# Performance work log

Measured on AMD Instinct MI355X. Metric: run time of the kernel, lower is better.

Reference implementation:

```python
import jax, jax.numpy as jnp
import numpy as np

D = 512          # feature dim
N = 4095         # context length
LMBD = 0.9       # eligibility-trace decay
DIM = 2 * D + 1  # 1025
CTX = N + 1      # 4096


def make_M(n: int, lmbd: float) -> jnp.ndarray:
    # M[row, col] = lmbd**(row-col) for col <= row < n, col < n; last row and
    # last column are all zero (M[-1, -1] explicitly zeroed in the original).
    i = jnp.arange(n, dtype=jnp.int32)
    diff = i[:, None] - i[None, :]
    core = jnp.where(diff >= 0, jnp.float32(lmbd) ** jnp.maximum(diff, 0).astype(jnp.float32), 0.0)
    M = jnp.zeros((n + 1, n + 1), dtype=jnp.float32)
    return M.at[:n, :n].set(core)


def setup_inputs() -> dict:
    key = jax.random.key(0)
    kz, kp, kq = jax.random.split(key, 3)
    Z = jax.random.normal(kz, (DIM, CTX), dtype=jnp.float32)
    # nn.Parameter(torch.empty(...)) is uninitialized in the source; use small
    # random values as stand-ins for trained parameters.
    P = jax.random.normal(kp, (DIM, DIM), dtype=jnp.float32) * 0.02
    Q = jax.random.normal(kq, (DIM, DIM), dtype=jnp.float32) * 0.02
    M = make_M(N, LMBD)
    return {"Z": Z, "P": P, "Q": Q, "M": M}


def reference(Z, P, Q, M):
    # X = Z^T Q Z : (CTX, CTX) bilinear attention scores
    X = jnp.einsum("dn,de,em->nm", Z, Q, Z)
    A = jax.nn.softmax(X, axis=-1)          # activation
    # Z + (1/n) * P @ Z @ M @ A ; contract left-to-right to keep (DIM, CTX) intermediates
    PZ = P @ Z                               # (DIM, CTX)
    PZM = PZ @ M                             # (DIM, CTX), M lower-tri decay
    return Z + (1.0 / N) * (PZM @ A)
```

## Files before the change

kernel.cpp:

```cpp
#include <hip/hip_runtime.h>


#define LMBD 0.9f
#define CTXN 4096
#define DIMN 1025
#define DP 1152

#define KSPLIT 832
#define PSTRIDE ((size_t)DP * CTXN)

typedef __bf16 bf16x8 __attribute__((ext_vector_type(8)));
typedef float f32x4 __attribute__((ext_vector_type(4)));
typedef long lx2 __attribute__((ext_vector_type(2)));

__device__ __forceinline__ unsigned short f2bf(float f) {
  union { float f; unsigned u; } v; v.f = f;
  unsigned r = v.u + 0x7FFFu + ((v.u >> 16) & 1u);
  return (unsigned short)(r >> 16);
}
__device__ __forceinline__ float bf2f(unsigned short h) {
  union { unsigned u; float f; } v; v.u = ((unsigned)h) << 16;
  return v.f;
}

__device__ __forceinline__ void gld_lds16(const void* g, void* l) {
  __builtin_amdgcn_global_load_lds(
      (const __attribute__((address_space(1))) unsigned int*)g,
      (__attribute__((address_space(3))) unsigned int*)l, 16, 0, 0);
}

template <int MODE, int TM, int TN>
__device__ __forceinline__ void gemm_body(
    const unsigned short* __restrict__ A, const unsigned short* __restrict__ B,
    void* __restrict__ Cout, int K, int lda, int ldb, int ldc, int bi, int bj,
    float* __restrict__ pmax, float* __restrict__ psum) {
  constexpr int CA = TM / 16, CB = TN / 16;
  constexpr int FI = TM / 32, FJ = TN / 32;
  __shared__ unsigned short sA[TM * 32];
  __shared__ unsigned short sB[TN * 32];
  const int tid = threadIdx.x;
  const int wave = tid >> 6;
  const int lane = tid & 63;
  const long i0 = (long)bi * TM;
  const long j0 = (long)bj * TN;
  const int wm = (wave & 1) * (TM / 2);
  const int wn = (wave >> 1) * (TN / 2);

  f32x4 acc[FI][FJ] = {};

  const int srow = lane >> 2;
  const int skc = (((lane & 3) - (lane >> 3)) & 3) * 8;
  const int mrow = lane & 15;
  const int slot = ((((lane >> 4) + (mrow >> 1)) & 3)) * 8;

  for (int k0 = 0; k0 < K; k0 += 32) {
    __syncthreads();
#pragma unroll
    for (int c = 0; c < CA / 4; ++c) {
      const int q = wave * (CA / 4) + c;
      gld_lds16(A + (i0 + q * 16 + srow) * (long)lda + k0 + skc, &sA[q * 512]);
    }
#pragma unroll
    for (int c = 0; c < CB / 4; ++c) {
      const int q = wave * (CB / 4) + c;
      gld_lds16(B + (j0 + q * 16 + srow) * (long)ldb + k0 + skc, &sB[q * 512]);
    }
    __syncthreads();
    bf16x8 af[FI], bfr[FJ];
#pragma unroll
    for (int i = 0; i < FI; ++i)
      af[i] = *(const bf16x8*)&sA[(wm + i * 16 + mrow) * 32 + slot];
#pragma unroll
    for (int j = 0; j < FJ; ++j)
      bfr[j] = *(const bf16x8*)&sB[(wn + j * 16 + mrow) * 32 + slot];
#pragma unroll
    for (int i = 0; i < FI; ++i)
#pragma unroll
      for (int j = 0; j < FJ; ++j)
        acc[i][j] =
            __builtin_amdgcn_mfma_f32_16x16x32_bf16(af[i], bfr[j], acc[i][j], 0, 0, 0);
  }

  const int lr = (lane >> 4) * 4;
  const int lc = lane & 15;
#pragma unroll
  for (int i = 0; i < FI; ++i) {
#pragma unroll
    for (int j = 0; j < FJ; ++j) {
#pragma unroll
      for (int r = 0; r < 4; ++r) {
        const long row = i0 + wm + i * 16 + lr + r;
        const long col = j0 + wn + j * 16 + lc;
        const float v = acc[i][j][r];
        if (MODE == 1) ((float*)Cout)[row * ldc + col] = v;
        else ((unsigned short*)Cout)[row * ldc + col] = f2bf(v);
      }
    }
  }

  if (MODE == 4) {
    float* sMax = (float*)sA;
    float* sSum = (float*)sB;
    const int k8 = (wave & 1) * 4 + (lane >> 4);
    __syncthreads();
#pragma unroll
    for (int j = 0; j < FJ; ++j) {
      float m = -1e30f;
#pragma unroll
      for (int i = 0; i < FI; ++i)
#pragma unroll
        for (int r = 0; r < 4; ++r) m = fmaxf(m, acc[i][j][r]);
      float s = 0.f;
#pragma unroll
      for (int i = 0; i < FI; ++i)
#pragma unroll
        for (int r = 0; r < 4; ++r) s += __expf(acc[i][j][r] - m);
      const int c = wn + j * 16 + lc;
      sMax[c * 8 + k8] = m;
      sSum[c * 8 + k8] = s;
    }
    __syncthreads();
    if (tid < 128) {
      float m = -1e30f;
#pragma unroll
      for (int k = 0; k < 8; ++k) m = fmaxf(m, sMax[tid * 8 + k]);
      float s = 0.f;
#pragma unroll
      for (int k = 0; k < 8; ++k) s += sSum[tid * 8 + k] * __expf(sMax[tid * 8 + k] - m);
      pmax[(size_t)bi * CTXN + j0 + tid] = m;
      psum[(size_t)bi * CTXN + j0 + tid] = s;
    }
  }
}

__global__ __launch_bounds__(256, 2) void gemm_xt(
    const unsigned short* __restrict__ QZT, const unsigned short* __restrict__ ZbT,
    unsigned short* __restrict__ XT, float* __restrict__ pmax,
    float* __restrict__ psum) {
  gemm_body<4, 128, 128>(QZT, ZbT, XT, DP, DP, DP, CTXN, blockIdx.x, blockIdx.y, pmax,
                         psum);
}

__global__ __launch_bounds__(256, 2) void gemm_dual(
    const unsigned short* __restrict__ ZbT, const unsigned short* __restrict__ Qb,
    unsigned short* __restrict__ QZT, const unsigned short* __restrict__ Pb,
    float* __restrict__ PZ) {
  const unsigned g = blockIdx.x;
  if (g < 576) {
    gemm_body<0, 128, 64>(ZbT, Qb, QZT, DP, DP, DP, DP, g & 31, g >> 5, nullptr,
                          nullptr);
  } else {
    const unsigned h = g - 576;
    gemm_body<1, 64, 128>(Pb, ZbT, PZ, DP, DP, DP, CTXN, h >> 5, h & 31, nullptr,
                          nullptr);
  }
}

__global__ __launch_bounds__(256, 2) void gemm_fp8_splitk(
    const unsigned char* __restrict__ A, const unsigned char* __restrict__ B,
    unsigned short* __restrict__ Cout) {
  __shared__ unsigned char sA[128 * 64];
  __shared__ unsigned char sB[128 * 64];
  const int tid = threadIdx.x;
  const int wave = tid >> 6;
  const int lane = tid & 63;
  const unsigned g = blockIdx.x;
  const unsigned bi = g / 160;
  const unsigned rem = g % 160;
  const unsigned bj = rem / 5;
  const unsigned bz = rem % 5;
  const long i0 = (long)bi * 128;
  const long j0 = (long)bj * 128;
  const int wm = (wave & 1) * 64;
  const int wn = (wave >> 1) * 64;
  const int kb = bz * KSPLIT;
  const int ke = min(CTXN, kb + KSPLIT);
  Cout += (size_t)bz * PSTRIDE;

  f32x4 acc[4][4] = {};
  const int srow = lane >> 2;
  const int skc = (((lane & 3) - (lane >> 3)) & 3) * 16;
  const int mrow = lane & 15;
  const int slot = ((((lane >> 4) + (mrow >> 1)) & 3)) * 16;

  for (int k0 = kb; k0 < ke; k0 += 64) {
    __syncthreads();
#pragma unroll
    for (int c = 0; c < 2; ++c) {
      const int q = wave * 2 + c;
      gld_lds16(A + (i0 + q * 16 + srow) * (long)CTXN + k0 + skc, &sA[q * 1024]);
      gld_lds16(B + (j0 + q * 16 + srow) * (long)CTXN + k0 + skc, &sB[q * 1024]);
    }
    __syncthreads();
    lx2 af[4], bfr[4];
#pragma unroll
    for (int i = 0; i < 4; ++i)
      af[i] = *(const lx2*)&sA[(wm + i * 16 + mrow) * 64 + slot];
#pragma unroll
    for (int j = 0; j < 4; ++j)
      bfr[j] = *(const lx2*)&sB[(wn + j * 16 + mrow) * 64 + slot];
#pragma unroll
    for (int i = 0; i < 4; ++i)
#pragma unroll
      for (int j = 0; j < 4; ++j) {
        acc[i][j] = __builtin_amdgcn_mfma_f32_16x16x32_fp8_fp8(af[i].x, bfr[j].x,
                                                               acc[i][j], 0, 0, 0);
        acc[i][j] = __builtin_amdgcn_mfma_f32_16x16x32_fp8_fp8(af[i].y, bfr[j].y,
                                                               acc[i][j], 0, 0, 0);
      }
  }

  const int lr = (lane >> 4) * 4;
  const int lc = lane & 15;
#pragma unroll
  for (int i = 0; i < 4; ++i)
#pragma unroll
    for (int j = 0; j < 4; ++j)
#pragma unroll
      for (int r = 0; r < 4; ++r) {
        const long row = i0 + wm + i * 16 + lr + r;
        if (row < DIMN)
          Cout[row * (long)CTXN + j0 + wn + j * 16 + lc] = f2bf(acc[i][j][r]);
      }
}

__global__ void reduce_kernel(const unsigned short* __restrict__ Pt,
                              const float* __restrict__ Z, float* __restrict__ out) {
  const size_t idx = ((size_t)blockIdx.x * 256 + threadIdx.x) * 4;
  float ax = 0.f, ay = 0.f, az = 0.f, aw = 0.f;
#pragma unroll
  for (int z = 0; z < 5; ++z) {
    const ushort4 v = *(const ushort4*)&Pt[(size_t)z * PSTRIDE + idx];
    ax += bf2f(v.x); ay += bf2f(v.y); az += bf2f(v.z); aw += bf2f(v.w);
  }
  const f32x4 zv = *(const f32x4*)&Z[idx];
  f32x4 o;
  o[0] = zv[0] + ax * 0.00390625f;
  o[1] = zv[1] + ay * 0.00390625f;
  o[2] = zv[2] + az * 0.00390625f;
  o[3] = zv[3] + aw * 0.00390625f;
  *(f32x4*)&out[idx] = o;
}

__global__ void pad_kernel(const float* __restrict__ Q, const float* __restrict__ P,
                           unsigned short* __restrict__ Qb,
                           unsigned short* __restrict__ Pb) {
  const int c = blockIdx.x * 128 + threadIdx.x;
  const int r = blockIdx.y;
  const float* src = blockIdx.z ? P : Q;
  unsigned short* dst = blockIdx.z ? Pb : Qb;
  float v = (r < DIMN && c < DIMN) ? src[(size_t)r * DIMN + c] : 0.f;
  dst[(size_t)r * DP + c] = f2bf(v);
}

__global__ void transZ_kernel(const float* __restrict__ Z, unsigned short* __restrict__ ZbT) {
  __shared__ float tile[32][33];
  const int n0 = blockIdx.x * 32, e0 = blockIdx.y * 32;
  const int tx = threadIdx.x, ty = threadIdx.y;
#pragma unroll
  for (int k = 0; k < 4; ++k) {
    const int e = e0 + ty + k * 8;
    tile[ty + k * 8][tx] = (e < DIMN) ? Z[(size_t)e * CTXN + n0 + tx] : 0.f;
  }
  __syncthreads();
#pragma unroll
  for (int k = 0; k < 4; ++k) {
    const int n = n0 + ty + k * 8;
    ZbT[(size_t)n * DP + e0 + tx] = f2bf(tile[tx][ty + k * 8]);
  }
}

__global__ void red2_kernel(const float* __restrict__ pmax, const float* __restrict__ psum,
                            float* __restrict__ rowmax, float* __restrict__ inv_l) {
  const int n = blockIdx.x * 256 + threadIdx.x;
  float M = -1e30f;
  for (int c = 0; c < 32; ++c) M = fmaxf(M, pmax[(size_t)c * CTXN + n]);
  float s = 0.f;
  for (int c = 0; c < 32; ++c)
    s += psum[(size_t)c * CTXN + n] * __expf(pmax[(size_t)c * CTXN + n] - M);
  rowmax[n] = M;
  inv_l[n] = 1.0f / (4095.0f * s);
}

__global__ void ew_kernel(const unsigned short* __restrict__ XT,
                          const float* __restrict__ rowmax, unsigned int* __restrict__ ET) {
  const size_t idx = ((size_t)blockIdx.x * 256 + threadIdx.x) * 4;
  const ushort4 v = *(const ushort4*)&XT[idx];
  const int n = (int)(idx & 4095);
  const float4 rm = *(const float4*)&rowmax[n];
  unsigned p = __builtin_amdgcn_cvt_pk_fp8_f32(__expf(bf2f(v.x) - rm.x),
                                               __expf(bf2f(v.y) - rm.y), 0, false);
  p = __builtin_amdgcn_cvt_pk_fp8_f32(__expf(bf2f(v.z) - rm.z),
                                      __expf(bf2f(v.w) - rm.w), p, true);
  ET[idx >> 2] = p;
}

__global__ __launch_bounds__(256) void scan_kernel(const float* __restrict__ PZ,
                                                   const float* __restrict__ inv_l,
                                                   unsigned char* __restrict__ out) {
  const int d = blockIdx.x;
  const int t = threadIdx.x;
  const float* row = PZ + (size_t)d * CTXN;
  float x[16];
#pragma unroll
  for (int q = 0; q < 4; ++q) {
    const float4 v = *(const float4*)&row[t * 16 + q * 4];
    x[q * 4 + 0] = v.x; x[q * 4 + 1] = v.y; x[q * 4 + 2] = v.z; x[q * 4 + 3] = v.w;
  }
  if (t == 255) x[15] = 0.f;
  float loc[16];
  float run = 0.f;
#pragma unroll
  for (int i = 15; i >= 0; --i) { run = run * LMBD + x[i]; loc[i] = run; }
  __shared__ float sF[256];
  float f = loc[0];
  sF[t] = f;
  __syncthreads();
  float mlt = 0.1853020188851841f;
  for (int step = 1; step < 256; step <<= 1) {
    const float other = (t + step < 256) ? sF[t + step] : 0.f;
    __syncthreads();
    f += mlt * other;
    mlt *= mlt;
    sF[t] = f;
    __syncthreads();
  }
  const float R = (t < 255) ? sF[t + 1] : 0.f;
  float il[16];
#pragma unroll
  for (int q = 0; q < 4; ++q) {
    const float4 v = *(const float4*)&inv_l[t * 16 + q * 4];
    il[q * 4 + 0] = v.x * 256.f; il[q * 4 + 1] = v.y * 256.f;
    il[q * 4 + 2] = v.z * 256.f; il[q * 4 + 3] = v.w * 256.f;
  }
  float o[16];
  float p = 1.f;
#pragma unroll
  for (int i = 15; i >= 0; --i) {
    p *= LMBD;
    o[i] = (loc[i] + p * R) * il[i];
  }
  unsigned w[4];
#pragma unroll
  for (int q = 0; q < 4; ++q) {
    unsigned pk = __builtin_amdgcn_cvt_pk_fp8_f32(o[q * 4 + 0], o[q * 4 + 1], 0, false);
    pk = __builtin_amdgcn_cvt_pk_fp8_f32(o[q * 4 + 2], o[q * 4 + 3], pk, true);
    w[q] = pk;
  }
  *(uint4*)&out[(size_t)d * CTXN + t * 16] = make_uint4(w[0], w[1], w[2], w[3]);
}

extern "C" void kernel_launch(void* const* d_in, const int* in_sizes, int n_in,
                              void* d_out, int out_size, void* d_ws, size_t ws_size,
                              hipStream_t stream) {
  const float* Z = (const float*)d_in[0];
  const float* P = (const float*)d_in[1];
  const float* Q = (const float*)d_in[2];

  char* ws = (char*)d_ws;
  size_t off = 0;
  auto alloc = [&](size_t bytes) {
    void* p = ws + off;
    off += (bytes + 255) & ~(size_t)255;
    return p;
  };
  unsigned char* ET   = (unsigned char*)alloc((size_t)CTXN * CTXN);
  unsigned char* PZMb = (unsigned char*)alloc((size_t)DP * CTXN);
  float* rowmax       = (float*)alloc((size_t)CTXN * 4);
  float* inv_l        = (float*)alloc((size_t)CTXN * 4);
  char* pool = (char*)alloc(0);
  unsigned short* ZbT = (unsigned short*)alloc((size_t)CTXN * DP * 2);
  unsigned short* QZT = (unsigned short*)alloc((size_t)CTXN * DP * 2);
  unsigned short* XT  = (unsigned short*)alloc((size_t)CTXN * CTXN * 2);
  float* PZ           = (float*)alloc((size_t)DP * CTXN * 4);
  unsigned short* Qb  = (unsigned short*)alloc((size_t)DP * DP * 2);
  unsigned short* Pb  = (unsigned short*)alloc((size_t)DP * DP * 2);
  float* pmax         = (float*)alloc((size_t)32 * CTXN * 4);
  float* psum         = (float*)alloc((size_t)32 * CTXN * 4);
  unsigned short* partials = (unsigned short*)pool;
  if (off > ws_size) return;

  pad_kernel<<<dim3(9, DP, 2), 128, 0, stream>>>(Q, P, Qb, Pb);
  transZ_kernel<<<dim3(128, 36), dim3(32, 8), 0, stream>>>(Z, ZbT);

  gemm_dual<<<1152, 256, 0, stream>>>(ZbT, Qb, QZT, Pb, PZ);

  gemm_xt<<<dim3(32, 32), 256, 0, stream>>>(QZT, ZbT, XT, pmax, psum);

  red2_kernel<<<16, 256, 0, stream>>>(pmax, psum, rowmax, inv_l);
  ew_kernel<<<16384, 256, 0, stream>>>(XT, rowmax, (unsigned int*)ET);

  scan_kernel<<<DP, 256, 0, stream>>>(PZ, inv_l, PZMb);

  gemm_fp8_splitk<<<1440, 256, 0, stream>>>(PZMb, ET, partials);
  reduce_kernel<<<4100, 256, 0, stream>>>(partials, Z, (float*)d_out);
}
```

Measured before the change: 274.8 us.

## Deepen bf16 GEMM K-tile, merge prep and ew/scan kernels, use 4-way split-K

The bf16 GEMM body now stages 64-wide K tiles in LDS with an 8-slot XOR-style swizzle and runs two MFMA sub-steps per barrier pair, halving the synchronisation count. pad and transpose kernels are fused into a single prep launch, and the elementwise exp and scan kernels are merged into one launch, cutting launch overhead. The FP8 split-K GEMM moves from 5 uneven splits to 4 equal splits of 1024, with a new block ordering, so the reduction reads fewer partials. LDS use per block doubles, which may reduce occupancy.

```diff
diff --git a/kernel.cpp b/kernel.cpp
--- a/kernel.cpp
+++ b/kernel.cpp
@@ -6,7 +6,7 @@
 #define DIMN 1025
 #define DP 1152
 
-#define KSPLIT 832
+#define KSPLIT 1024
 #define PSTRIDE ((size_t)DP * CTXN)
 
 typedef __bf16 bf16x8 __attribute__((ext_vector_type(8)));
@@ -34,10 +34,9 @@
     const unsigned short* __restrict__ A, const unsigned short* __restrict__ B,
     void* __restrict__ Cout, int K, int lda, int ldb, int ldc, int bi, int bj,
     float* __restrict__ pmax, float* __restrict__ psum) {
-  constexpr int CA = TM / 16, CB = TN / 16;
   constexpr int FI = TM / 32, FJ = TN / 32;
-  __shared__ unsigned short sA[TM * 32];
-  __shared__ unsigned short sB[TN * 32];
+  __shared__ unsigned short sA[TM * 64];
+  __shared__ unsigned short sB[TN * 64];
   const int tid = threadIdx.x;
   const int wave = tid >> 6;
   const int lane = tid & 63;
@@ -48,37 +47,46 @@
 
   f32x4 acc[FI][FJ] = {};
 
-  const int srow = lane >> 2;
-  const int skc = (((lane & 3) - (lane >> 3)) & 3) * 8;
+  const int srow8 = lane >> 3;
+  const int s = lane & 7;
   const int mrow = lane & 15;
-  const int slot = ((((lane >> 4) + (mrow >> 1)) & 3)) * 8;
-
-  for (int k0 = 0; k0 < K; k0 += 32) {
-    __syncthreads();
-#pragma unroll
-    for (int c = 0; c < CA / 4; ++c) {
-      const int q = wave * (CA / 4) + c;
-      gld_lds16(A + (i0 + q * 16 + srow) * (long)lda + k0 + skc, &sA[q * 512]);
-    }
-#pragma unroll
-    for (int c = 0; c < CB / 4; ++c) {
-      const int q = wave * (CB / 4) + c;
-      gld_lds16(B + (j0 + q * 16 + srow) * (long)ldb + k0 + skc, &sB[q * 512]);
-    }
-    __syncthreads();
-    bf16x8 af[FI], bfr[FJ];
-#pragma unroll
-    for (int i = 0; i < FI; ++i)
-      af[i] = *(const bf16x8*)&sA[(wm + i * 16 + mrow) * 32 + slot];
-#pragma unroll
-    for (int j = 0; j < FJ; ++j)
-      bfr[j] = *(const bf16x8*)&sB[(wn + j * 16 + mrow) * 32 + slot];
-#pragma unroll
-    for (int i = 0; i < FI; ++i)
+  const int q2 = lane >> 4;
+  const int swz = mrow >> 1;
+
+  for (int k0 = 0; k0 < K; k0 += 64) {
+    __syncthreads();
+#pragma unroll
+    for (int c = 0; c < TM / 32; ++c) {
+      const int q = wave * (TM / 32) + c;
+      const int r = q * 8 + srow8;
+      const int gk = (s - ((r & 15) >> 1)) & 7;
+      gld_lds16(A + (i0 + r) * (long)lda + k0 + gk * 8, &sA[q * 512]);
+    }
+#pragma unroll
+    for (int c = 0; c < TN / 32; ++c) {
+      const int q = wave * (TN / 32) + c;
+      const int r = q * 8 + srow8;
+      const int gk = (s - ((r & 15) >> 1)) & 7;
+      gld_lds16(B + (j0 + r) * (long)ldb + k0 + gk * 8, &sB[q * 512]);
+    }
+    __syncthreads();
+#pragma unroll
+    for (int kk = 0; kk < 2; ++kk) {
+      const int slot = ((kk * 4 + q2) + swz) & 7;
+      bf16x8 af[FI], bfr[FJ];
+#pragma unroll
+      for (int i = 0; i < FI; ++i)
+        af[i] = *(const bf16x8*)&sA[(wm + i * 16 + mrow) * 64 + slot * 8];
 #pragma unroll
       for (int j = 0; j < FJ; ++j)
-        acc[i][j] =
-            __builtin_amdgcn_mfma_f32_16x16x32_bf16(af[i], bfr[j], acc[i][j], 0, 0, 0);
+        bfr[j] = *(const bf16x8*)&sB[(wn + j * 16 + mrow) * 64 + slot * 8];
+#pragma unroll
+      for (int i = 0; i < FI; ++i)
+#pragma unroll
+        for (int j = 0; j < FJ; ++j)
+          acc[i][j] =
+              __builtin_amdgcn_mfma_f32_16x16x32_bf16(af[i], bfr[j], acc[i][j], 0, 0, 0);
+    }
   }
 
   const int lr = (lane >> 4) * 4;
@@ -110,25 +118,25 @@
       for (int i = 0; i < FI; ++i)
 #pragma unroll
         for (int r = 0; r < 4; ++r) m = fmaxf(m, acc[i][j][r]);
-      float s = 0.f;
+      float sv = 0.f;
 #pragma unroll
       for (int i = 0; i < FI; ++i)
 #pragma unroll
-        for (int r = 0; r < 4; ++r) s += __expf(acc[i][j][r] - m);
+        for (int r = 0; r < 4; ++r) sv += __expf(acc[i][j][r] - m);
       const int c = wn + j * 16 + lc;
       sMax[c * 8 + k8] = m;
-      sSum[c * 8 + k8] = s;
+      sSum[c * 8 + k8] = sv;
     }
     __syncthreads();
     if (tid < 128) {
       float m = -1e30f;
 #pragma unroll
       for (int k = 0; k < 8; ++k) m = fmaxf(m, sMax[tid * 8 + k]);
-      float s = 0.f;
-#pragma unroll
-      for (int k = 0; k < 8; ++k) s += sSum[tid * 8 + k] * __expf(sMax[tid * 8 + k] - m);
+      float sv = 0.f;
+#pragma unroll
+      for (int k = 0; k < 8; ++k) sv += sSum[tid * 8 + k] * __expf(sMax[tid * 8 + k] - m);
       pmax[(size_t)bi * CTXN + j0 + tid] = m;
-      psum[(size_t)bi * CTXN + j0 + tid] = s;
+      psum[(size_t)bi * CTXN + j0 + tid] = sv;
     }
   }
 }
@@ -165,16 +173,15 @@
   const int wave = tid >> 6;
   const int lane = tid & 63;
   const unsigned g = blockIdx.x;
-  const unsigned bi = g / 160;
-  const unsigned rem = g % 160;
-  const unsigned bj = rem / 5;
-  const unsigned bz = rem % 5;
+  const unsigned bj = g & 31;
+  const unsigned t = g >> 5;
+  const unsigned bi = t >> 2;
+  const unsigned bz = t & 3;
   const long i0 = (long)bi * 128;
   const long j0 = (long)bj * 128;
   const int wm = (wave & 1) * 64;
   const int wn = (wave >> 1) * 64;
   const int kb = bz * KSPLIT;
-  const int ke = min(CTXN, kb + KSPLIT);
   Cout += (size_t)bz * PSTRIDE;
 
   f32x4 acc[4][4] = {};
@@ -183,7 +190,7 @@
   const int mrow = lane & 15;
   const int slot = ((((lane >> 4) + (mrow >> 1)) & 3)) * 16;
 
-  for (int k0 = kb; k0 < ke; k0 += 64) {
+  for (int k0 = kb; k0 < kb + KSPLIT; k0 += 64) {
     __syncthreads();
 #pragma unroll
     for (int c = 0; c < 2; ++c) {
@@ -229,7 +236,7 @@
   const size_t idx = ((size_t)blockIdx.x * 256 + threadIdx.x) * 4;
   float ax = 0.f, ay = 0.f, az = 0.f, aw = 0.f;
 #pragma unroll
-  for (int z = 0; z < 5; ++z) {
+  for (int z = 0; z < 4; ++z) {
     const ushort4 v = *(const ushort4*)&Pt[(size_t)z * PSTRIDE + idx];
     ax += bf2f(v.x); ay += bf2f(v.y); az += bf2f(v.z); aw += bf2f(v.w);
   }
@@ -242,31 +249,42 @@
   *(f32x4*)&out[idx] = o;
 }
 
-__global__ void pad_kernel(const float* __restrict__ Q, const float* __restrict__ P,
-                           unsigned short* __restrict__ Qb,
-                           unsigned short* __restrict__ Pb) {
-  const int c = blockIdx.x * 128 + threadIdx.x;
-  const int r = blockIdx.y;
-  const float* src = blockIdx.z ? P : Q;
-  unsigned short* dst = blockIdx.z ? Pb : Qb;
-  float v = (r < DIMN && c < DIMN) ? src[(size_t)r * DIMN + c] : 0.f;
-  dst[(size_t)r * DP + c] = f2bf(v);
-}
-
-__global__ void transZ_kernel(const float* __restrict__ Z, unsigned short* __restrict__ ZbT) {
+__global__ void prep_kernel(const float* __restrict__ Z, const float* __restrict__ Q,
+                            const float* __restrict__ P,
+                            unsigned short* __restrict__ ZbT,
+                            unsigned short* __restrict__ Qb,
+                            unsigned short* __restrict__ Pb) {
   __shared__ float tile[32][33];
-  const int n0 = blockIdx.x * 32, e0 = blockIdx.y * 32;
-  const int tx = threadIdx.x, ty = threadIdx.y;
-#pragma unroll
-  for (int k = 0; k < 4; ++k) {
-    const int e = e0 + ty + k * 8;
-    tile[ty + k * 8][tx] = (e < DIMN) ? Z[(size_t)e * CTXN + n0 + tx] : 0.f;
-  }
-  __syncthreads();
-#pragma unroll
-  for (int k = 0; k < 4; ++k) {
-    const int n = n0 + ty + k * 8;
-    ZbT[(size_t)n * DP + e0 + tx] = f2bf(tile[tx][ty + k * 8]);
+  const unsigned g = blockIdx.x;
+  const int tid = threadIdx.x;
+  if (g < 4608) {
+    const int n0 = (g & 127) * 32, e0 = (g >> 7) * 32;
+    const int tx = tid & 31, ty = tid >> 5;
+#pragma unroll
+    for (int k = 0; k < 4; ++k) {
+      const int e = e0 + ty + k * 8;
+      tile[ty + k * 8][tx] = (e < DIMN) ? Z[(size_t)e * CTXN + n0 + tx] : 0.f;
+    }
+    __syncthreads();
+#pragma unroll
+    for (int k = 0; k < 4; ++k) {
+      const int n = n0 + ty + k * 8;
+      ZbT[(size_t)n * DP + e0 + tx] = f2bf(tile[tx][ty + k * 8]);
+    }
+  } else {
+    const unsigned id2 = g - 4608;
+    const int mat = id2 >= 1296;
+    const float* src = mat ? P : Q;
+    unsigned short* dst = mat ? Pb : Qb;
+    const unsigned e0 = (id2 - (mat ? 1296u : 0u)) * 1024u + tid * 4u;
+    const unsigned r = e0 / 1152u;
+    const unsigned c = e0 - r * 1152u;
+    ushort4 o;
+    o.x = (r < DIMN && c + 0 < DIMN) ? f2bf(src[(size_t)r * DIMN + c + 0]) : 0;
+    o.y = (r < DIMN && c + 1 < DIMN) ? f2bf(src[(size_t)r * DIMN + c + 1]) : 0;
+    o.z = (r < DIMN && c + 2 < DIMN) ? f2bf(src[(size_t)r * DIMN + c + 2]) : 0;
+    o.w = (r < DIMN && c + 3 < DIMN) ? f2bf(src[(size_t)r * DIMN + c + 3]) : 0;
+    *(ushort4*)&dst[(size_t)r * DP + c] = o;
   }
 }
 
@@ -282,24 +300,26 @@
   inv_l[n] = 1.0f / (4095.0f * s);
 }
 
-__global__ void ew_kernel(const unsigned short* __restrict__ XT,
-                          const float* __restrict__ rowmax, unsigned int* __restrict__ ET) {
-  const size_t idx = ((size_t)blockIdx.x * 256 + threadIdx.x) * 4;
-  const ushort4 v = *(const ushort4*)&XT[idx];
-  const int n = (int)(idx & 4095);
-  const float4 rm = *(const float4*)&rowmax[n];
-  unsigned p = __builtin_amdgcn_cvt_pk_fp8_f32(__expf(bf2f(v.x) - rm.x),
-                                               __expf(bf2f(v.y) - rm.y), 0, false);
-  p = __builtin_amdgcn_cvt_pk_fp8_f32(__expf(bf2f(v.z) - rm.z),
-                                      __expf(bf2f(v.w) - rm.w), p, true);
-  ET[idx >> 2] = p;
-}
-
-__global__ __launch_bounds__(256) void scan_kernel(const float* __restrict__ PZ,
-                                                   const float* __restrict__ inv_l,
-                                                   unsigned char* __restrict__ out) {
-  const int d = blockIdx.x;
+__global__ __launch_bounds__(256) void ewscan_kernel(
+    const unsigned short* __restrict__ XT, const float* __restrict__ rowmax,
+    unsigned int* __restrict__ ET, const float* __restrict__ PZ,
+    const float* __restrict__ inv_l, unsigned char* __restrict__ PZMb) {
+  __shared__ float sF[256];
+  const unsigned g = blockIdx.x;
   const int t = threadIdx.x;
+  if (g >= 1152) {
+    const size_t idx = ((size_t)(g - 1152) * 256 + t) * 4;
+    const ushort4 v = *(const ushort4*)&XT[idx];
+    const int n = (int)(idx & 4095);
+    const float4 rm = *(const float4*)&rowmax[n];
+    unsigned p = __builtin_amdgcn_cvt_pk_fp8_f32(__expf(bf2f(v.x) - rm.x),
+                                                 __expf(bf2f(v.y) - rm.y), 0, false);
+    p = __builtin_amdgcn_cvt_pk_fp8_f32(__expf(bf2f(v.z) - rm.z),
+                                        __expf(bf2f(v.w) - rm.w), p, true);
+    ET[idx >> 2] = p;
+    return;
+  }
+  const int d = g;
   const float* row = PZ + (size_t)d * CTXN;
   float x[16];
 #pragma unroll
@@ -312,7 +332,6 @@
   float run = 0.f;
 #pragma unroll
   for (int i = 15; i >= 0; --i) { run = run * LMBD + x[i]; loc[i] = run; }
-  __shared__ float sF[256];
   float f = loc[0];
   sF[t] = f;
   __syncthreads();
@@ -347,7 +366,7 @@
     pk = __builtin_amdgcn_cvt_pk_fp8_f32(o[q * 4 + 2], o[q * 4 + 3], pk, true);
     w[q] = pk;
   }
-  *(uint4*)&out[(size_t)d * CTXN + t * 16] = make_uint4(w[0], w[1], w[2], w[3]);
+  *(uint4*)&PZMb[(size_t)d * CTXN + t * 16] = make_uint4(w[0], w[1], w[2], w[3]);
 }
 
 extern "C" void kernel_launch(void* const* d_in, const int* in_sizes, int n_in,
@@ -380,18 +399,17 @@
   unsigned short* partials = (unsigned short*)pool;
   if (off > ws_size) return;
 
-  pad_kernel<<<dim3(9, DP, 2), 128, 0, stream>>>(Q, P, Qb, Pb);
-  transZ_kernel<<<dim3(128, 36), dim3(32, 8), 0, stream>>>(Z, ZbT);
+  prep_kernel<<<7200, 256, 0, stream>>>(Z, Q, P, ZbT, Qb, Pb);
 
   gemm_dual<<<1152, 256, 0, stream>>>(ZbT, Qb, QZT, Pb, PZ);
 
   gemm_xt<<<dim3(32, 32), 256, 0, stream>>>(QZT, ZbT, XT, pmax, psum);
 
   red2_kernel<<<16, 256, 0, stream>>>(pmax, psum, rowmax, inv_l);
-  ew_kernel<<<16384, 256, 0, stream>>>(XT, rowmax, (unsigned int*)ET);
-
-  scan_kernel<<<DP, 256, 0, stream>>>(PZ, inv_l, PZMb);
-
-  gemm_fp8_splitk<<<1440, 256, 0, stream>>>(PZMb, ET, partials);
+
+  ewscan_kernel<<<17536, 256, 0, stream>>>(XT, rowmax, (unsigned int*)ET, PZ, inv_l,
+                                           PZMb);
+
+  gemm_fp8_splitk<<<1152, 256, 0, stream>>>(PZMb, ET, partials);
   reduce_kernel<<<4100, 256, 0, stream>>>(partials, Z, (float*)d_out);
 }
```

Result: faster. 247.9 us (-9.8%).
